# Kernel tuning notes

Hardware: AMD Instinct MI355X
Metric: run time of the kernel (lower is better)

## Reference

```python
import jax, jax.numpy as jnp
import numpy as np

H = 16  # num_heads

def _toroidal_bias(S, dtype):
    # float mask: +1.0 at (i, (i-1)%S), (i,i), (i, (i+1)%S); PyTorch ADDS float attn_mask to scores
    eye = jnp.eye(S, dtype=dtype)
    return eye + jnp.roll(eye, 1, axis=1) + jnp.roll(eye, -1, axis=1)

def setup_inputs() -> dict:
    key = jax.random.key(0)
    ks = jax.random.split(key, 7)
    E = 1024
    S, B = 2048, 2
    sc = 0.02
    return {
        "x": jax.random.normal(ks[0], (S, B, E), dtype=jnp.float32),
        "w_tor": jax.random.normal(ks[1], (E, E), dtype=jnp.float32) * sc,
        "b_tor": jax.random.normal(ks[2], (E,), dtype=jnp.float32) * sc,
        "in_proj_w": jax.random.normal(ks[3], (3 * E, E), dtype=jnp.float32) * sc,
        "in_proj_b": jax.random.normal(ks[4], (3 * E,), dtype=jnp.float32) * sc,
        "out_w": jax.random.normal(ks[5], (E, E), dtype=jnp.float32) * sc,
        "out_b": jax.random.normal(ks[6], (E,), dtype=jnp.float32) * sc,
    }

def reference(x, w_tor, b_tor, in_proj_w, in_proj_b, out_w, out_b):
    S, B, E = x.shape
    hd = E // H
    scale = 1.0 / jnp.sqrt(jnp.asarray(hd, dtype=x.dtype))
    # toroidal projection, then fused in_proj (self-attention: q=k=v=x_toroidal)
    xt = x @ w_tor.T + b_tor                      # (S,B,E)
    qkv = xt @ in_proj_w.T + in_proj_b            # (S,B,3E)
    q, k, v = jnp.split(qkv, 3, axis=-1)
    def to_heads(t):
        return t.reshape(S, B, H, hd).transpose(1, 2, 0, 3)  # (B,H,S,hd)
    q, k, v = to_heads(q), to_heads(k), to_heads(v)
    bias = _toroidal_bias(S, x.dtype)             # (S,S) additive float mask
    scores = jnp.einsum('bhqd,bhkd->bhqk', q * scale, k) + bias
    attn = jax.nn.softmax(scores, axis=-1)
    o = jnp.einsum('bhqk,bhkd->bhqd', attn, v)    # (B,H,S,hd)
    o = o.transpose(2, 0, 1, 3).reshape(S, B, E)
    return o @ out_w.T + out_b
```

## Files before the change

### kernel.cpp

```cpp
#include <hip/hip_runtime.h>

#define S_LEN 2048
#define NB    2
#define EMB   1024
#define NH    16
#define HD    64

typedef __bf16 bf16_t;
typedef bf16_t bf16x8 __attribute__((ext_vector_type(8)));
typedef bf16_t bf16x4v __attribute__((ext_vector_type(4)));
typedef float  f32x4  __attribute__((ext_vector_type(4)));
typedef float  f32x16 __attribute__((ext_vector_type(16)));

#define L2E 1.44269504f

__device__ __forceinline__ void g2l16(const void* g, void* l) {
    auto gp = reinterpret_cast<const unsigned int __attribute__((address_space(1)))*>(
        reinterpret_cast<uintptr_t>(g));
    auto lp = reinterpret_cast<unsigned int __attribute__((address_space(3)))*>(
        reinterpret_cast<uintptr_t>(l));
    __builtin_amdgcn_global_load_lds(gp, lp, 16, 0, 0);
}

__device__ __forceinline__ unsigned int pk2(float a, float b) {
    union { unsigned int u; bf16_t h[2]; } r;
    r.h[0] = (bf16_t)a; r.h[1] = (bf16_t)b;
    return r.u;
}

__global__ __launch_bounds__(256) void cast4_f32_bf16(
    const float* __restrict__ s0, bf16_t* __restrict__ d0,
    const float* __restrict__ s1, bf16_t* __restrict__ d1,
    const float* __restrict__ s2, bf16_t* __restrict__ d2,
    const float* __restrict__ s3, bf16_t* __restrict__ d3)
{
    long i = (long)blockIdx.x * 256 + threadIdx.x;
    const float* s; bf16_t* d; long off;
    if (i < 1048576)      { s = s0; d = d0; off = i; }
    else if (i < 1310720) { s = s1; d = d1; off = i - 1048576; }
    else if (i < 2097152) { s = s2; d = d2; off = i - 1310720; }
    else                  { s = s3; d = d3; off = i - 2097152; }
    float4 v = ((const float4*)s)[off];
    bf16x4v o;
    o[0] = (bf16_t)v.x; o[1] = (bf16_t)v.y; o[2] = (bf16_t)v.z; o[3] = (bf16_t)v.w;
    *(bf16x4v*)(d + off * 4) = o;
}

template<int TN, int MODE, int MT, int NT>
__global__ __launch_bounds__(256) void gemm_bt_bf16(
    const bf16_t* __restrict__ A, const bf16_t* __restrict__ W,
    const float* __restrict__ bias, void* __restrict__ Cout,
    bf16_t* __restrict__ Qp, bf16_t* __restrict__ Kp, bf16_t* __restrict__ Vtp,
    int M, int N, int K)
{
    constexpr int MB = (TN == 128) ? 4 : 2;
    __shared__ __align__(16) bf16_t As[2][128 * 32];
    __shared__ __align__(16) bf16_t Bs[2][TN * 32];

    const int tid  = threadIdx.x;
    const int lane = tid & 63;
    const int w    = tid >> 6;
    const int lm   = lane & 15;
    const int lq   = lane >> 4;

    constexpr int MR = MT / 4;
    constexpr int NR = NT / 2;
    const int bid  = blockIdx.x;
    const int xcd  = bid & 7;
    const int idx  = bid >> 3;
    const long m0  = (long)((xcd >> 1) * MR + idx / NR) * 128;
    const long n0  = (long)((xcd & 1) * NR + idx % NR) * TN;

    const int wm0  = (TN == 128) ? (w >> 1) * 64 : w * 32;
    const int wn0  = (TN == 128) ? (w & 1) * 64 : 0;

    f32x4 acc[MB][4];
#pragma unroll
    for (int i = 0; i < MB; ++i)
#pragma unroll
        for (int j = 0; j < 4; ++j) acc[i][j] = (f32x4){0.f, 0.f, 0.f, 0.f};

    auto stage = [&](int k0, int buf) {
        bf16_t* asb = &As[buf][0];
        bf16_t* bsb = &Bs[buf][0];
#pragma unroll
        for (int j = 0; j < 2; ++j) {
            int a   = (w * 2 + j) * 64 + lane;
            int row = a >> 2;
            int c   = (a & 3) ^ ((row >> 1) & 3);
            g2l16(A + (m0 + row) * K + k0 + c * 8, asb + (w * 2 + j) * 512);
        }
#pragma unroll
        for (int j = 0; j < TN / 64; ++j) {
            int a   = (w * (TN / 64) + j) * 64 + lane;
            int row = a >> 2;
            int c   = (a & 3) ^ ((row >> 1) & 3);
            g2l16(W + (n0 + row) * K + k0 + c * 8, bsb + (w * (TN / 64) + j) * 512);
        }
    };

    stage(0, 0);
    for (int k0 = 0; k0 < K; k0 += 32) {
        const int cur = (k0 >> 5) & 1;
        asm volatile("s_waitcnt vmcnt(0)" ::: "memory");
        __syncthreads();
        if (k0 + 32 < K) stage(k0 + 32, cur ^ 1);

        bf16x8 af[MB], bfr[4];
#pragma unroll
        for (int mb = 0; mb < MB; ++mb) {
            int r = wm0 + mb * 16 + lm;
            af[mb] = *(const bf16x8*)&As[cur][r * 32 + ((lq ^ ((r >> 1) & 3)) << 3)];
        }
#pragma unroll
        for (int nb = 0; nb < 4; ++nb) {
            int r = wn0 + nb * 16 + lm;
            bfr[nb] = *(const bf16x8*)&Bs[cur][r * 32 + ((lq ^ ((r >> 1) & 3)) << 3)];
        }
#pragma unroll
        for (int mb = 0; mb < MB; ++mb)
#pragma unroll
            for (int nb = 0; nb < 4; ++nb)
                acc[mb][nb] = __builtin_amdgcn_mfma_f32_16x16x32_bf16(
                    af[mb], bfr[nb], acc[mb][nb], 0, 0, 0);
    }

    float b4[4];
#pragma unroll
    for (int nb = 0; nb < 4; ++nb) b4[nb] = bias[n0 + wn0 + nb * 16 + lm];

    if (MODE == 2) {
#pragma unroll
        for (int mb = 0; mb < MB; ++mb) {
            const long mbase = m0 + wm0 + mb * 16 + lq * 4;
#pragma unroll
            for (int nb = 0; nb < 4; ++nb) {
                int n    = (int)n0 + wn0 + nb * 16 + lm;
                int sec  = n >> 10;
                int nloc = n & 1023;
                int h    = nloc >> 6;
                int d    = nloc & 63;
                if (sec == 2) {
                    int s0 = (int)(mbase >> 1);
                    int sp = (s0 & ~12) | ((s0 & 4) << 1) | ((s0 & 8) >> 1);
#pragma unroll
                    for (int rp = 0; rp < 2; ++rp) {
                        int bh = rp * 16 + h;
                        unsigned int pkv = pk2(acc[mb][nb][rp]     + b4[nb],
                                               acc[mb][nb][rp + 2] + b4[nb]);
                        *(unsigned int*)&Vtp[((size_t)(bh * 64 + d)) * S_LEN + sp] = pkv;
                    }
                } else {
#pragma unroll
                    for (int r = 0; r < 4; ++r) {
                        long m  = mbase + r;
                        int  s  = (int)(m >> 1), b = (int)(m & 1);
                        int  bh = b * 16 + h;
                        float v = acc[mb][nb][r] + b4[nb];
                        if (sec == 0) {
                            Qp[((size_t)(bh * S_LEN + s)) * 64 + d] =
                                (bf16_t)(v * (0.125f * L2E));
                        } else {
                            Kp[((size_t)(bh * S_LEN + s)) * 64 + d] = (bf16_t)v;
                        }
                    }
                }
            }
        }
    } else {
#pragma unroll
        for (int mb = 0; mb < MB; ++mb) {
#pragma unroll
            for (int r = 0; r < 4; ++r) {
                long m = m0 + wm0 + mb * 16 + lq * 4 + r;
#pragma unroll
                for (int nb = 0; nb < 4; ++nb) {
                    int n   = (int)n0 + wn0 + nb * 16 + lm;
                    float v = acc[mb][nb][r] + b4[nb];
                    if (MODE == 0) ((float*)Cout)[m * N + n] = v;
                    else           ((bf16_t*)Cout)[m * N + n] = (bf16_t)v;
                }
            }
        }
    }
}

__global__ __launch_bounds__(256, 2) void attn_mfma(
    const bf16_t* __restrict__ Qb, const bf16_t* __restrict__ Kb,
    const bf16_t* __restrict__ Vtb, bf16_t* __restrict__ O)
{
    __shared__ __align__(16) bf16_t Ks[2][8 * 512];
    __shared__ __align__(16) bf16_t Vts[2][8 * 512];
    __shared__ __align__(16) float  Lw4[4][32];

    const int tid  = threadIdx.x;
    const int lane = tid & 63;
    const int w    = tid >> 6;
    const int bid  = blockIdx.x;
    const int bh   = ((bid & 7) << 2) | (bid >> 7);
    const int qt   = (bid >> 3) & 15;
    const int l5   = lane & 31;
    const int hi   = lane >> 5;

    const int rsub = lane >> 3;
    const int csw  = (lane & 7) ^ rsub;
    int cc[4];
#pragma unroll
    for (int i = 0; i < 4; ++i) cc[i] = ((2 * i + hi) ^ (l5 & 7)) * 8;

    const bf16_t* qrow = Qb + ((size_t)bh * S_LEN + qt * 128 + w * 32 + l5) * 64 + hi * 8;
    bf16x8 qf[4];
#pragma unroll
    for (int ds = 0; ds < 4; ++ds) qf[ds] = *(const bf16x8*)(qrow + ds * 16);

    f32x16 oacc[2];
#pragma unroll
    for (int dh = 0; dh < 2; ++dh)
#pragma unroll
        for (int i = 0; i < 16; ++i) oacc[dh][i] = 0.f;
    float plsum = 0.f;

    auto stageKV = [&](int kt, int buf) {
        bf16_t* ksb = &Ks[buf][0];
        bf16_t* vsb = &Vts[buf][0];
        const bf16_t* kg = Kb + ((size_t)bh * S_LEN + kt * 64) * 64;
        const bf16_t* vg = Vtb + (size_t)bh * 64 * S_LEN + kt * 64;
#pragma unroll
        for (int j = 0; j < 2; ++j) {
            int i = w * 2 + j;
            g2l16(kg + (size_t)(i * 8 + rsub) * 64 + csw * 8,    ksb + i * 512);
            g2l16(vg + (size_t)(i * 8 + rsub) * S_LEN + csw * 8, vsb + i * 512);
        }
    };

    stageKV(0, 0);
    for (int kt = 0; kt < 32; ++kt) {
        const int cur = kt & 1;
        asm volatile("s_waitcnt vmcnt(0)" ::: "memory");
        __syncthreads();
        if (kt < 31) stageKV(kt + 1, cur ^ 1);

        f32x16 sacc[2];
        __builtin_amdgcn_s_setprio(1);
#pragma unroll
        for (int kh = 0; kh < 2; ++kh) {
#pragma unroll
            for (int i = 0; i < 16; ++i) sacc[kh][i] = 0.f;
#pragma unroll
            for (int ds = 0; ds < 4; ++ds) {
                bf16x8 kf = *(const bf16x8*)&Ks[cur][(kh * 32 + l5) * 64 + cc[ds]];
                sacc[kh] = __builtin_amdgcn_mfma_f32_32x32x16_bf16(kf, qf[ds], sacc[kh], 0, 0, 0);
            }
        }
        __builtin_amdgcn_s_setprio(0);

        int ktd = (kt - 2 * qt) & 31;
        if (ktd <= 2 || ktd == 31) {
            int q = qt * 128 + w * 32 + l5;
#pragma unroll
            for (int kh = 0; kh < 2; ++kh)
#pragma unroll
                for (int r = 0; r < 16; ++r) {
                    int key  = kt * 64 + kh * 32 + (r & 3) + 8 * (r >> 2) + 4 * hi;
                    int diff = (key - q) & (S_LEN - 1);
                    if (diff <= 1 || diff == S_LEN - 1) sacc[kh][r] += L2E;
                }
        }

        float pv[2][16];
#pragma unroll
        for (int kh = 0; kh < 2; ++kh)
#pragma unroll
            for (int i = 0; i < 16; ++i) {
                pv[kh][i] = __builtin_amdgcn_exp2f(sacc[kh][i]);
                plsum += pv[kh][i];
            }

        bf16x8 pf[4];
#pragma unroll
        for (int ks = 0; ks < 4; ++ks) {
            const int kh = ks >> 1, m = ks & 1;
#pragma unroll
            for (int e = 0; e < 8; ++e)
                pf[ks][e] = (bf16_t)pv[kh][(e & 3) + 8 * m + 4 * (e >> 2)];
        }

        __builtin_amdgcn_s_setprio(1);
#pragma unroll
        for (int dh = 0; dh < 2; ++dh) {
#pragma unroll
            for (int ks = 0; ks < 4; ++ks) {
                bf16x8 vf = *(const bf16x8*)&Vts[cur][(dh * 32 + l5) * 64 + cc[ks]];
                oacc[dh] = __builtin_amdgcn_mfma_f32_32x32x16_bf16(pf[ks], vf, oacc[dh], 0, 0, 0);
            }
        }
        __builtin_amdgcn_s_setprio(0);
    }

    plsum += __shfl_xor(plsum, 32, 64);
    if (hi == 0) Lw4[w][l5] = plsum;

    float inv16[16];
#pragma unroll
    for (int g = 0; g < 4; ++g) {
        f32x4 lv = *(const f32x4*)&Lw4[w][8 * g + 4 * hi];
#pragma unroll
        for (int e = 0; e < 4; ++e) inv16[g * 4 + e] = 1.0f / lv[e];
    }

    const int b = bh >> 4, h = bh & 15;
#pragma unroll
    for (int dh = 0; dh < 2; ++dh)
#pragma unroll
        for (int r = 0; r < 16; ++r) {
            int qrel = (r & 3) + 8 * (r >> 2) + 4 * hi;
            int s = qt * 128 + w * 32 + qrel;
            O[((size_t)(s * NB + b)) * EMB + h * 64 + dh * 32 + l5] =
                (bf16_t)(oacc[dh][r] * inv16[r]);
        }
}

extern "C" void kernel_launch(void* const* d_in, const int* in_sizes, int n_in,
                              void* d_out, int out_size, void* d_ws, size_t ws_size,
                              hipStream_t stream)
{
    const float* x         = (const float*)d_in[0];
    const float* w_tor     = (const float*)d_in[1];
    const float* b_tor     = (const float*)d_in[2];
    const float* in_proj_w = (const float*)d_in[3];
    const float* in_proj_b = (const float*)d_in[4];
    const float* out_w     = (const float*)d_in[5];
    const float* out_b     = (const float*)d_in[6];
    float* out = (float*)d_out;

    const int M = S_LEN * NB;

    char* base = (char*)d_ws;
    bf16_t* xb    = (bf16_t*)(base);
    bf16_t* wtorb = (bf16_t*)(base + ( 8ull << 20));
    bf16_t* ipwb  = (bf16_t*)(base + (10ull << 20));
    bf16_t* outwb = (bf16_t*)(base + (16ull << 20));
    bf16_t* xtb   = (bf16_t*)(base + (18ull << 20));
    bf16_t* Kb    = (bf16_t*)(base + (26ull << 20));
    bf16_t* Vtb   = (bf16_t*)(base + (34ull << 20));
    bf16_t* Qb    = xb;
    bf16_t* Ob    = xtb;

    cast4_f32_bf16<<<dim3(9216), 256, 0, stream>>>(
        x, xb, w_tor, wtorb, in_proj_w, ipwb, out_w, outwb);

    gemm_bt_bf16<64, 1, 32, 16><<<dim3(512), 256, 0, stream>>>(
        xb, wtorb, b_tor, xtb, nullptr, nullptr, nullptr, M, EMB, EMB);

    gemm_bt_bf16<128, 2, 32, 24><<<dim3(768), 256, 0, stream>>>(
        xtb, ipwb, in_proj_b, nullptr, Qb, Kb, Vtb, M, 3 * EMB, EMB);

    attn_mfma<<<dim3(32 * 16), 256, 0, stream>>>(Qb, Kb, Vtb, Ob);

    gemm_bt_bf16<64, 0, 32, 16><<<dim3(512), 256, 0, stream>>>(
        Ob, outwb, out_b, out, nullptr, nullptr, nullptr, M, EMB, EMB);
}
```

Baseline: 208.8 us.

## Deepen GEMM K-tile to 64 and widen QKV tile to 192 columns

The GEMM kernel now stages 64-wide K slices per iteration instead of 32, which halves the number of barrier and wait cycles per block. Shared memory moves to a dynamic allocation so tile sizes can vary. The QKV projection uses 128x192 tiles across 512 blocks instead of 128x128 across 768, so each loaded A tile is reused by more columns. The trade-off is more LDS and registers per block, which may lower occupancy even with the added launch bound of 2 blocks.

```diff
diff --git a/kernel.cpp b/kernel.cpp
--- a/kernel.cpp
+++ b/kernel.cpp
@@ -47,15 +47,18 @@
 }
 
 template<int TN, int MODE, int MT, int NT>
-__global__ __launch_bounds__(256) void gemm_bt_bf16(
+__global__ __launch_bounds__(256, 2) void gemm_bt_bf16(
     const bf16_t* __restrict__ A, const bf16_t* __restrict__ W,
     const float* __restrict__ bias, void* __restrict__ Cout,
     bf16_t* __restrict__ Qp, bf16_t* __restrict__ Kp, bf16_t* __restrict__ Vtp,
     int M, int N, int K)
 {
-    constexpr int MB = (TN == 128) ? 4 : 2;
-    __shared__ __align__(16) bf16_t As[2][128 * 32];
-    __shared__ __align__(16) bf16_t Bs[2][TN * 32];
+    constexpr int MB  = (TN == 64) ? 2 : 4;
+    constexpr int NBn = (TN == 64) ? 4 : TN / 32;
+    constexpr int BI  = TN / 64;
+    extern __shared__ __align__(16) char smem[];
+    bf16_t* AsB = (bf16_t*)smem;
+    bf16_t* BsB = (bf16_t*)(smem + 32768);
 
     const int tid  = threadIdx.x;
     const int lane = tid & 63;
@@ -71,70 +74,81 @@
     const long m0  = (long)((xcd >> 1) * MR + idx / NR) * 128;
     const long n0  = (long)((xcd & 1) * NR + idx % NR) * TN;
 
-    const int wm0  = (TN == 128) ? (w >> 1) * 64 : w * 32;
-    const int wn0  = (TN == 128) ? (w & 1) * 64 : 0;
-
-    f32x4 acc[MB][4];
+    const int wm0  = (TN == 64) ? w * 32 : (w >> 1) * 64;
+    const int wn0  = (TN == 64) ? 0 : (w & 1) * (TN / 2);
+
+    f32x4 acc[MB][NBn];
 #pragma unroll
     for (int i = 0; i < MB; ++i)
 #pragma unroll
-        for (int j = 0; j < 4; ++j) acc[i][j] = (f32x4){0.f, 0.f, 0.f, 0.f};
-
-    auto stage = [&](int k0, int buf) {
-        bf16_t* asb = &As[buf][0];
-        bf16_t* bsb = &Bs[buf][0];
-#pragma unroll
-        for (int j = 0; j < 2; ++j) {
-            int a   = (w * 2 + j) * 64 + lane;
+        for (int j = 0; j < NBn; ++j) acc[i][j] = (f32x4){0.f, 0.f, 0.f, 0.f};
+
+    auto stage = [&](int t, int buf) {
+        const int k0 = t * 64;
+        bf16_t* asb = AsB + buf * 8192;
+#pragma unroll
+        for (int j = 0; j < 4; ++j) {
+            int kh = j >> 1, jj = j & 1;
+            int a   = (w * 2 + jj) * 64 + lane;
             int row = a >> 2;
             int c   = (a & 3) ^ ((row >> 1) & 3);
-            g2l16(A + (m0 + row) * K + k0 + c * 8, asb + (w * 2 + j) * 512);
-        }
-#pragma unroll
-        for (int j = 0; j < TN / 64; ++j) {
-            int a   = (w * (TN / 64) + j) * 64 + lane;
+            g2l16(A + (m0 + row) * K + k0 + kh * 32 + c * 8,
+                  asb + kh * 4096 + (w * 2 + jj) * 512);
+        }
+        bf16_t* bsb = BsB + buf * (TN * 64);
+#pragma unroll
+        for (int j = 0; j < 2 * BI; ++j) {
+            int kh = j / BI, jj = j % BI;
+            int a   = (w * BI + jj) * 64 + lane;
             int row = a >> 2;
             int c   = (a & 3) ^ ((row >> 1) & 3);
-            g2l16(W + (n0 + row) * K + k0 + c * 8, bsb + (w * (TN / 64) + j) * 512);
+            g2l16(W + (n0 + row) * K + k0 + kh * 32 + c * 8,
+                  bsb + kh * (TN * 32) + (w * BI + jj) * 512);
         }
     };
 
     stage(0, 0);
-    for (int k0 = 0; k0 < K; k0 += 32) {
-        const int cur = (k0 >> 5) & 1;
+    const int NTILES = K / 64;
+    for (int t = 0; t < NTILES; ++t) {
+        const int cur = t & 1;
         asm volatile("s_waitcnt vmcnt(0)" ::: "memory");
         __syncthreads();
-        if (k0 + 32 < K) stage(k0 + 32, cur ^ 1);
-
-        bf16x8 af[MB], bfr[4];
-#pragma unroll
-        for (int mb = 0; mb < MB; ++mb) {
-            int r = wm0 + mb * 16 + lm;
-            af[mb] = *(const bf16x8*)&As[cur][r * 32 + ((lq ^ ((r >> 1) & 3)) << 3)];
-        }
-#pragma unroll
-        for (int nb = 0; nb < 4; ++nb) {
-            int r = wn0 + nb * 16 + lm;
-            bfr[nb] = *(const bf16x8*)&Bs[cur][r * 32 + ((lq ^ ((r >> 1) & 3)) << 3)];
-        }
-#pragma unroll
-        for (int mb = 0; mb < MB; ++mb)
-#pragma unroll
-            for (int nb = 0; nb < 4; ++nb)
-                acc[mb][nb] = __builtin_amdgcn_mfma_f32_16x16x32_bf16(
-                    af[mb], bfr[nb], acc[mb][nb], 0, 0, 0);
+        if (t + 1 < NTILES) stage(t + 1, cur ^ 1);
+
+#pragma unroll
+        for (int kh = 0; kh < 2; ++kh) {
+            const bf16_t* Ab = AsB + cur * 8192 + kh * 4096;
+            const bf16_t* Bb = BsB + cur * (TN * 64) + kh * (TN * 32);
+            bf16x8 af[MB], bfr[NBn];
+#pragma unroll
+            for (int mb = 0; mb < MB; ++mb) {
+                int r = wm0 + mb * 16 + lm;
+                af[mb] = *(const bf16x8*)&Ab[r * 32 + ((lq ^ ((r >> 1) & 3)) << 3)];
+            }
+#pragma unroll
+            for (int nb = 0; nb < NBn; ++nb) {
+                int r = wn0 + nb * 16 + lm;
+                bfr[nb] = *(const bf16x8*)&Bb[r * 32 + ((lq ^ ((r >> 1) & 3)) << 3)];
+            }
+#pragma unroll
+            for (int mb = 0; mb < MB; ++mb)
+#pragma unroll
+                for (int nb = 0; nb < NBn; ++nb)
+                    acc[mb][nb] = __builtin_amdgcn_mfma_f32_16x16x32_bf16(
+                        af[mb], bfr[nb], acc[mb][nb], 0, 0, 0);
+        }
     }
 
-    float b4[4];
-#pragma unroll
-    for (int nb = 0; nb < 4; ++nb) b4[nb] = bias[n0 + wn0 + nb * 16 + lm];
+    float b4[NBn];
+#pragma unroll
+    for (int nb = 0; nb < NBn; ++nb) b4[nb] = bias[n0 + wn0 + nb * 16 + lm];
 
     if (MODE == 2) {
 #pragma unroll
         for (int mb = 0; mb < MB; ++mb) {
             const long mbase = m0 + wm0 + mb * 16 + lq * 4;
 #pragma unroll
-            for (int nb = 0; nb < 4; ++nb) {
+            for (int nb = 0; nb < NBn; ++nb) {
                 int n    = (int)n0 + wn0 + nb * 16 + lm;
                 int sec  = n >> 10;
                 int nloc = n & 1023;
@@ -174,7 +188,7 @@
             for (int r = 0; r < 4; ++r) {
                 long m = m0 + wm0 + mb * 16 + lq * 4 + r;
 #pragma unroll
-                for (int nb = 0; nb < 4; ++nb) {
+                for (int nb = 0; nb < NBn; ++nb) {
                     int n   = (int)n0 + wn0 + nb * 16 + lm;
                     float v = acc[mb][nb][r] + b4[nb];
                     if (MODE == 0) ((float*)Cout)[m * N + n] = v;
@@ -346,17 +360,22 @@
     bf16_t* Qb    = xb;
     bf16_t* Ob    = xtb;
 
+    const int lds64  = 32768 + 64 * 256;
+    const int lds192 = 32768 + 192 * 256;
+    hipFuncSetAttribute((const void*)gemm_bt_bf16<192, 2, 32, 16>,
+                        hipFuncAttributeMaxDynamicSharedMemorySize, lds192);
+
     cast4_f32_bf16<<<dim3(9216), 256, 0, stream>>>(
         x, xb, w_tor, wtorb, in_proj_w, ipwb, out_w, outwb);
 
-    gemm_bt_bf16<64, 1, 32, 16><<<dim3(512), 256, 0, stream>>>(
+    gemm_bt_bf16<64, 1, 32, 16><<<dim3(512), 256, lds64, stream>>>(
         xb, wtorb, b_tor, xtb, nullptr, nullptr, nullptr, M, EMB, EMB);
 
-    gemm_bt_bf16<128, 2, 32, 24><<<dim3(768), 256, 0, stream>>>(
+    gemm_bt_bf16<192, 2, 32, 16><<<dim3(512), 256, lds192, stream>>>(
         xtb, ipwb, in_proj_b, nullptr, Qb, Kb, Vtb, M, 3 * EMB, EMB);
 
     attn_mfma<<<dim3(32 * 16), 256, 0, stream>>>(Qb, Kb, Vtb, Ob);
 
-    gemm_bt_bf16<64, 0, 32, 16><<<dim3(512), 256, 0, stream>>>(
+    gemm_bt_bf16<64, 0, 32, 16><<<dim3(512), 256, lds64, stream>>>(
         Ob, outwb, out_b, out, nullptr, nullptr, nullptr, M, EMB, EMB);
 }
```

Measured after the change: 196.8 us. 5.8% less time.
